# Kernel tuning notes

Measured on AMD Instinct MI355X. Metric: run time of the kernel, lower is better.

The kernel has to match this reference:

```python
import jax, jax.numpy as jnp
import numpy as np

B, N, D, H, DK, DI = 64, 256, 1024, 8, 64, 2048
NEG = -1e9
SCALE = 1.0 / np.sqrt(DK).astype(np.float32)


def _ln(x, s, b, eps=1e-5):
    m = jnp.mean(x, axis=-1, keepdims=True)
    v = jnp.var(x, axis=-1, keepdims=True)
    return (x - m) * jax.lax.rsqrt(v + eps) * s + b


def _glat_basic(x, mask, npm, wq, wk, wv, wo, bo, ls1, lb1, w1, b1, w2, b2, ls2, lb2):
    # mask: [B,1,N,N] bool, True = blocked
    b, n, d = x.shape
    q = (x @ wq).reshape(b, n, H, DK).transpose(0, 2, 1, 3)  # [B,H,N,DK]
    k = (x @ wk).reshape(b, n, H, DK).transpose(0, 2, 1, 3)
    v = (x @ wv).reshape(b, n, H, DK).transpose(0, 2, 1, 3)
    scores = jnp.einsum('bhqd,bhkd->bhqk', q, k) * SCALE
    scores = jnp.where(mask, NEG, scores)
    attn = jax.nn.softmax(scores, axis=-1)
    out = jnp.einsum('bhqk,bhkd->bhqd', attn, v)
    out = out.transpose(0, 2, 1, 3).reshape(b, n, H * DK)
    out = out @ wo + bo
    out = _ln(out + x, ls1, lb1)           # attn residual + layernorm
    out = out * npm                         # non_pad_mask
    h = jax.nn.relu(out @ w1 + b1) @ w2 + b2
    out2 = _ln(h + out, ls2, lb2) * npm     # FFN residual + layernorm + mask
    return out2


def setup_inputs():
    key = jax.random.key(0)
    ks = jax.random.split(key, 40)
    p = lambda i, shape: jax.random.normal(ks[i], shape, jnp.float32) * 0.02
    inp = {
        'x': jax.random.normal(ks[0], (B, N, D), jnp.float32),
        'adj': jax.random.randint(ks[1], (B, N, N), 0, 2).astype(jnp.int32),
        'non_pad_mask': jnp.ones((B, N, 1), jnp.float32),
        'slf_attn_mask': jnp.zeros((B, N, N), jnp.int32),
    }
    i = 2
    for t in ('g', 'l'):
        inp[f'wq_{t}'] = p(i, (D, H * DK)); i += 1
        inp[f'wk_{t}'] = p(i, (D, H * DK)); i += 1
        inp[f'wv_{t}'] = p(i, (D, H * DK)); i += 1
        inp[f'wo_{t}'] = p(i, (H * DK, D)); i += 1
        inp[f'bo_{t}'] = jnp.zeros((D,), jnp.float32)
        inp[f'ln1s_{t}'] = jnp.ones((D,), jnp.float32)
        inp[f'ln1b_{t}'] = jnp.zeros((D,), jnp.float32)
        inp[f'w1_{t}'] = p(i, (D, DI)); i += 1
        inp[f'b1_{t}'] = jnp.zeros((DI,), jnp.float32)
        inp[f'w2_{t}'] = p(i, (DI, D)); i += 1
        inp[f'b2_{t}'] = jnp.zeros((D,), jnp.float32)
        inp[f'ln2s_{t}'] = jnp.ones((D,), jnp.float32)
        inp[f'ln2b_{t}'] = jnp.zeros((D,), jnp.float32)
    inp['fc_w'] = p(i, (2 * D, D)); i += 1
    inp['fc_b'] = jnp.zeros((D,), jnp.float32)
    return inp


def reference(x, adj, non_pad_mask, slf_attn_mask,
              wq_g, wk_g, wv_g, wo_g, bo_g, ln1s_g, ln1b_g, w1_g, b1_g, w2_g, b2_g, ln2s_g, ln2b_g,
              wq_l, wk_l, wv_l, wo_l, bo_l, ln1s_l, ln1b_l, w1_l, b1_l, w2_l, b2_l, ln2s_l, ln2b_l,
              fc_w, fc_b):
    pad_mask = (slf_attn_mask[:, None, :, :] != 0)            # [B,1,N,N]
    local_mask = pad_mask | (adj[:, None, :, :] == 0)         # local: only attend along edges
    x_g = _glat_basic(x, pad_mask, non_pad_mask,
                      wq_g, wk_g, wv_g, wo_g, bo_g, ln1s_g, ln1b_g,
                      w1_g, b1_g, w2_g, b2_g, ln2s_g, ln2b_g)
    x_l = _glat_basic(x, local_mask, non_pad_mask,
                      wq_l, wk_l, wv_l, wo_l, bo_l, ln1s_l, ln1b_l,
                      w1_l, b1_l, w2_l, b2_l, ln2s_l, ln2b_l)
    out = jnp.concatenate([x_g, x_l], axis=-1) @ fc_w + fc_b
    return out
```

## Files before the change

kernel.cpp:

```cpp
#include <hip/hip_runtime.h>


typedef unsigned short u16;
typedef unsigned long long u64;
typedef __bf16 bf16_t;
typedef bf16_t bf16x8 __attribute__((ext_vector_type(8)));
typedef float  f32x4  __attribute__((ext_vector_type(4)));
typedef u16    u16x8  __attribute__((ext_vector_type(8)));
typedef u16    u16x4  __attribute__((ext_vector_type(4)));

__device__ __forceinline__ float bf2f(u16 u){
  union { unsigned int i; float f; } c; c.i = ((unsigned int)u) << 16; return c.f;
}
__device__ __forceinline__ u16 f2bf(float f){
  union { float f; unsigned int u; } c; c.f = f;
  unsigned int u = c.u;
  unsigned int r = (u + 0x7fffu + ((u >> 16) & 1u)) >> 16;
  return (u16)r;
}

__device__ __forceinline__ void gl16(const u16* g, u16* l){
  __builtin_amdgcn_global_load_lds(
      (const __attribute__((address_space(1))) void*)g,
      (__attribute__((address_space(3))) void*)l, 16, 0, 0);
}

__global__ __launch_bounds__(256) void zero_out(float* out, int n){
  for (int i = blockIdx.x * 256 + threadIdx.x; i < n; i += 256 * 4096) out[i] = 0.f;
}

__global__ __launch_bounds__(256) void cvt_bf16(
    const float* __restrict__ in, u16* __restrict__ out)
{
  const size_t i = ((size_t)blockIdx.x * 256 + threadIdx.x) * 8;
  f32x4 a = *(const f32x4*)&in[i];
  f32x4 b = *(const f32x4*)&in[i + 4];
  u16x8 o;
  #pragma unroll
  for (int j = 0; j < 4; ++j){ o[j] = f2bf(a[j]); o[4+j] = f2bf(b[j]); }
  *(u16x8*)&out[i] = o;
}

__global__ __launch_bounds__(256) void transpose_w(
    const float* __restrict__ src, u16* __restrict__ dst, int K, int N, int dstOff)
{
  __shared__ u16 tile[32][33];
  const int bk = blockIdx.x * 32, bn = blockIdx.y * 32;
  const int t = threadIdx.x;
  const int r = t >> 5, c = t & 31;
  #pragma unroll
  for (int p = 0; p < 4; ++p)
    tile[r + p*8][c] = f2bf(src[(size_t)(bk + r + p*8) * N + bn + c]);
  __syncthreads();
  #pragma unroll
  for (int p = 0; p < 4; ++p)
    dst[(size_t)(dstOff + bn + r + p*8) * K + bk + c] = tile[c][r + p*8];
}

template<int RELU, int OF32, int ACC>
__global__ __launch_bounds__(512, 2) void gemm256(
    const u16* __restrict__ A0, const u16* __restrict__ A1,
    int Astride, int ksplit,
    const u16* __restrict__ BT, int Bld, int M, int N, int K,
    const float* __restrict__ bias, void* __restrict__ outv, int out_ld)
{
  __shared__ u16 lds[2*32768];
  const int tid  = threadIdx.x;
  const int lane = tid & 63;
  const int wid  = tid >> 6;
  const int wm = wid >> 2, wn = wid & 3;
  const int l15 = lane & 15, l4 = lane >> 4;
  const int m0 = blockIdx.x * 256, n0 = blockIdx.y * 256;

  f32x4 acc[8][4];
  #pragma unroll
  for (int i = 0; i < 8; ++i)
    #pragma unroll
    for (int j = 0; j < 4; ++j)
      acc[i][j] = (f32x4){0.f, 0.f, 0.f, 0.f};

  const int s0 = tid, s1 = tid + 512;
  const int r0 = s0 >> 3, g0 = (s0 & 7) ^ (r0 & 7);
  const int r1 = s1 >> 3, g1 = (s1 & 7) ^ (r1 & 7);

  const int nt = K >> 6;

  auto stageA = [&](int kt, int h, int buf){
    const int kb = kt * 64;
    const u16* Ab = A0; int kl = kb;
    if (kb >= ksplit){ Ab = A1; kl = kb - ksplit; }
    u16* dst = &lds[buf*32768 + h*8192];
    gl16(&Ab[(size_t)(m0 + h*128 + r0) * Astride + kl + g0*8], &dst[s0*8]);
    gl16(&Ab[(size_t)(m0 + h*128 + r1) * Astride + kl + g1*8], &dst[s1*8]);
  };
  auto stageB = [&](int kt, int h, int buf){
    const int kb = kt * 64;
    u16* dst = &lds[buf*32768 + 16384 + h*8192];
    gl16(&BT[(size_t)(n0 + h*128 + r0) * Bld + kb + g0*8], &dst[s0*8]);
    gl16(&BT[(size_t)(n0 + h*128 + r1) * Bld + kb + g1*8], &dst[s1*8]);
  };
  auto lda = [&](int i, int kc, int buf) -> bf16x8 {
    const int r = wm*128 + i*16 + l15;
    const int c = (kc*4 + l4) ^ (r & 7);
    return *(const bf16x8*)&lds[buf*32768 + r*64 + c*8];
  };
  auto ldb = [&](int j, int kc, int buf) -> bf16x8 {
    const int r = wn*64 + j*16 + l15;
    const int c = (kc*4 + l4) ^ (r & 7);
    return *(const bf16x8*)&lds[buf*32768 + 16384 + r*64 + c*8];
  };

  stageA(0, 0, 0); stageA(0, 1, 0); stageB(0, 0, 0); stageB(0, 1, 0);

  for (int t = 0; t < nt; ++t){
    const int buf = t & 1, nbuf = buf ^ 1;
    const bool pf = (t + 1 < nt);
    if (pf){
      stageA(t+1, 0, nbuf);
      asm volatile("s_waitcnt vmcnt(2)" ::: "memory");
    } else {
      asm volatile("s_waitcnt vmcnt(0)" ::: "memory");
    }
    __builtin_amdgcn_sched_barrier(0);
    __builtin_amdgcn_s_barrier();
    __builtin_amdgcn_sched_barrier(0);

    bf16x8 a_[4][2], b_[2][2];
    #pragma unroll
    for (int i = 0; i < 4; ++i){ a_[i][0] = lda(i, 0, buf); a_[i][1] = lda(i, 1, buf); }
    #pragma unroll
    for (int j = 0; j < 2; ++j){ b_[j][0] = ldb(j, 0, buf); b_[j][1] = ldb(j, 1, buf); }
    if (pf) stageA(t+1, 1, nbuf);
    __builtin_amdgcn_s_setprio(1);
    #pragma unroll
    for (int i = 0; i < 4; ++i)
      #pragma unroll
      for (int j = 0; j < 2; ++j){
        acc[i][j] = __builtin_amdgcn_mfma_f32_16x16x32_bf16(a_[i][0], b_[j][0], acc[i][j], 0,0,0);
        acc[i][j] = __builtin_amdgcn_mfma_f32_16x16x32_bf16(a_[i][1], b_[j][1], acc[i][j], 0,0,0);
      }
    __builtin_amdgcn_s_setprio(0);
    #pragma unroll
    for (int j = 0; j < 2; ++j){ b_[j][0] = ldb(2+j, 0, buf); b_[j][1] = ldb(2+j, 1, buf); }
    if (pf) stageB(t+1, 0, nbuf);
    __builtin_amdgcn_s_setprio(1);
    #pragma unroll
    for (int i = 0; i < 4; ++i)
      #pragma unroll
      for (int j = 0; j < 2; ++j){
        acc[i][2+j] = __builtin_amdgcn_mfma_f32_16x16x32_bf16(a_[i][0], b_[j][0], acc[i][2+j], 0,0,0);
        acc[i][2+j] = __builtin_amdgcn_mfma_f32_16x16x32_bf16(a_[i][1], b_[j][1], acc[i][2+j], 0,0,0);
      }
    __builtin_amdgcn_s_setprio(0);
    #pragma unroll
    for (int i = 0; i < 4; ++i){ a_[i][0] = lda(4+i, 0, buf); a_[i][1] = lda(4+i, 1, buf); }
    if (pf) stageB(t+1, 1, nbuf);
    __builtin_amdgcn_s_setprio(1);
    #pragma unroll
    for (int i = 0; i < 4; ++i)
      #pragma unroll
      for (int j = 0; j < 2; ++j){
        acc[4+i][2+j] = __builtin_amdgcn_mfma_f32_16x16x32_bf16(a_[i][0], b_[j][0], acc[4+i][2+j], 0,0,0);
        acc[4+i][2+j] = __builtin_amdgcn_mfma_f32_16x16x32_bf16(a_[i][1], b_[j][1], acc[4+i][2+j], 0,0,0);
      }
    __builtin_amdgcn_s_setprio(0);
    #pragma unroll
    for (int j = 0; j < 2; ++j){ b_[j][0] = ldb(j, 0, buf); b_[j][1] = ldb(j, 1, buf); }
    __builtin_amdgcn_s_setprio(1);
    #pragma unroll
    for (int i = 0; i < 4; ++i)
      #pragma unroll
      for (int j = 0; j < 2; ++j){
        acc[4+i][j] = __builtin_amdgcn_mfma_f32_16x16x32_bf16(a_[i][0], b_[j][0], acc[4+i][j], 0,0,0);
        acc[4+i][j] = __builtin_amdgcn_mfma_f32_16x16x32_bf16(a_[i][1], b_[j][1], acc[4+i][j], 0,0,0);
      }
    __builtin_amdgcn_s_setprio(0);

    __builtin_amdgcn_sched_barrier(0);
    __builtin_amdgcn_s_barrier();
    __builtin_amdgcn_sched_barrier(0);
  }

  const int rb = m0 + wm*128 + l4*4;
  const int cb = n0 + wn*64 + l15;
  #pragma unroll
  for (int i = 0; i < 8; ++i){
    #pragma unroll
    for (int j = 0; j < 4; ++j){
      const int col = cb + j*16;
      const float badd = bias ? bias[col] : 0.f;
      #pragma unroll
      for (int r = 0; r < 4; ++r){
        const int row = rb + i*16 + r;
        float y = acc[i][j][r] + badd;
        if (RELU) y = y > 0.f ? y : 0.f;
        if (OF32){
          float* po = &((float*)outv)[(size_t)row * out_ld + col];
          if (ACC) y += *po;
          *po = y;
        } else {
          u16* po = &((u16*)outv)[(size_t)row * out_ld + col];
          if (ACC) y += bf2f(*po);
          *po = f2bf(y);
        }
      }
    }
  }
}

__global__ __launch_bounds__(256) void mask_pack(
    const int* __restrict__ slf, const int* __restrict__ adj,
    u64* __restrict__ mb_g, u64* __restrict__ mb_l)
{
  const int idx  = blockIdx.x * 4 + (threadIdx.x >> 6);
  const int lane = threadIdx.x & 63;
  const size_t mi = (size_t)(idx >> 2) * 256 + (size_t)(idx & 3) * 64 + lane;
  const bool g = slf[mi] != 0;
  const bool l = g || (adj[mi] == 0);
  const u64 bg = __ballot(g);
  const u64 bl = __ballot(l);
  if (lane == 0){ mb_g[idx] = bg; mb_l[idx] = bl; }
}

__global__ __launch_bounds__(256) void attn_mfma(
    const u16* __restrict__ qkv, const u64* __restrict__ mb,
    int boff, u16* __restrict__ out)
{
  __shared__ u16 kbuf[64*64];
  __shared__ u16 vtbuf[64*64];
  __shared__ u16 pbuf[4][32*64];

  const int b_loc = blockIdx.x >> 4;
  const int h     = (blockIdx.x >> 1) & 7;
  const int qt    = blockIdx.x & 1;
  const int b     = boff + b_loc;
  const int t     = threadIdx.x;
  const int w     = t >> 6, lane = t & 63;
  const int l15   = lane & 15, l4 = lane >> 4;

  bf16x8 qf[2][2];
  {
    const int rbase = b_loc*256 + qt*128 + w*32;
    #pragma unroll
    for (int i = 0; i < 2; ++i)
      #pragma unroll
      for (int kc = 0; kc < 2; ++kc)
        qf[i][kc] = *(const bf16x8*)&qkv[(size_t)(rbase + i*16 + l15)*1536 + h*64 + kc*32 + l4*8];
  }

  f32x4 acc_o[2][4];
  float m_[2][4], l_[2][4];
  #pragma unroll
  for (int i = 0; i < 2; ++i){
    #pragma unroll
    for (int j = 0; j < 4; ++j) acc_o[i][j] = (f32x4){0.f,0.f,0.f,0.f};
    #pragma unroll
    for (int r = 0; r < 4; ++r){ m_[i][r] = -1e30f; l_[i][r] = 0.f; }
  }

  for (int c = 0; c < 4; ++c){
    __syncthreads();
    {
      const int kr = t >> 2, dg = (t & 3) * 16;
      const size_t rbase = (size_t)(b_loc*256 + c*64 + kr)*1536 + h*64 + dg;
      u16x8 k0 = *(const u16x8*)&qkv[rbase + 512];
      u16x8 k1 = *(const u16x8*)&qkv[rbase + 512 + 8];
      u16x8 v0 = *(const u16x8*)&qkv[rbase + 1024];
      u16x8 v1 = *(const u16x8*)&qkv[rbase + 1024 + 8];
      const int sw = (kr & 7) << 3;
      *(u16x8*)&kbuf[kr*64 + (dg ^ sw)]       = k0;
      *(u16x8*)&kbuf[kr*64 + ((dg + 8) ^ sw)] = k1;
      #pragma unroll
      for (int e = 0; e < 8; ++e){
        const int d0 = dg + e, d1 = dg + 8 + e;
        vtbuf[d0*64 + (kr ^ ((d0 & 7) << 3))] = v0[e];
        vtbuf[d1*64 + (kr ^ ((d1 & 7) << 3))] = v1[e];
      }
    }
    __syncthreads();

    bf16x8 kfr[4][2];
    #pragma unroll
    for (int jb = 0; jb < 4; ++jb){
      const int key = jb*16 + l15;
      const int sw = (key & 7) << 3;
      #pragma unroll
      for (int kc = 0; kc < 2; ++kc)
        kfr[jb][kc] = *(const bf16x8*)&kbuf[key*64 + ((kc*32 + l4*8) ^ sw)];
    }
    f32x4 s_[2][4];
    #pragma unroll
    for (int i = 0; i < 2; ++i)
      #pragma unroll
      for (int jb = 0; jb < 4; ++jb){
        f32x4 a = (f32x4){0.f,0.f,0.f,0.f};
        a = __builtin_amdgcn_mfma_f32_16x16x32_bf16(qf[i][0], kfr[jb][0], a, 0,0,0);
        a = __builtin_amdgcn_mfma_f32_16x16x32_bf16(qf[i][1], kfr[jb][1], a, 0,0,0);
        s_[i][jb] = a;
      }

    #pragma unroll
    for (int i = 0; i < 2; ++i){
      #pragma unroll
      for (int r = 0; r < 4; ++r){
        const int prow = i*16 + l4*4 + r;
        const int qrow = qt*128 + w*32 + prow;
        const u64 bits = mb[((size_t)b*256 + qrow)*4 + c];
        float sv[4];
        #pragma unroll
        for (int jb = 0; jb < 4; ++jb){
          float xv = s_[i][jb][r] * 0.125f;
          if ((bits >> (jb*16 + l15)) & 1ull) xv = -1e9f;
          sv[jb] = xv;
        }
        float mx = fmaxf(fmaxf(sv[0], sv[1]), fmaxf(sv[2], sv[3]));
        #pragma unroll
        for (int d = 1; d < 16; d <<= 1)
          mx = fmaxf(mx, __shfl_xor(mx, d, 64));
        const float mnew = fmaxf(m_[i][r], mx);
        const float corr = __expf(m_[i][r] - mnew);
        m_[i][r] = mnew;
        float ps = 0.f;
        const int swp = (prow & 7) << 3;
        #pragma unroll
        for (int jb = 0; jb < 4; ++jb){
          const float p = __expf(sv[jb] - mnew);
          ps += p;
          pbuf[w][prow*64 + ((jb*16 + l15) ^ swp)] = f2bf(p);
        }
        #pragma unroll
        for (int d = 1; d < 16; d <<= 1)
          ps += __shfl_xor(ps, d, 64);
        l_[i][r] = l_[i][r] * corr + ps;
        #pragma unroll
        for (int j2 = 0; j2 < 4; ++j2) acc_o[i][j2][r] *= corr;
      }
    }

    bf16x8 vfr[4][2];
    #pragma unroll
    for (int j2 = 0; j2 < 4; ++j2){
      const int dim = j2*16 + l15;
      const int sw = (dim & 7) << 3;
      #pragma unroll
      for (int kc = 0; kc < 2; ++kc)
        vfr[j2][kc] = *(const bf16x8*)&vtbuf[dim*64 + ((kc*32 + l4*8) ^ sw)];
    }
    #pragma unroll
    for (int i = 0; i < 2; ++i){
      const int prow = i*16 + l15;
      const int swp = (prow & 7) << 3;
      bf16x8 pa0 = *(const bf16x8*)&pbuf[w][prow*64 + ((l4*8) ^ swp)];
      bf16x8 pa1 = *(const bf16x8*)&pbuf[w][prow*64 + ((32 + l4*8) ^ swp)];
      #pragma unroll
      for (int j2 = 0; j2 < 4; ++j2){
        acc_o[i][j2] = __builtin_amdgcn_mfma_f32_16x16x32_bf16(pa0, vfr[j2][0], acc_o[i][j2], 0,0,0);
        acc_o[i][j2] = __builtin_amdgcn_mfma_f32_16x16x32_bf16(pa1, vfr[j2][1], acc_o[i][j2], 0,0,0);
      }
    }
  }

  #pragma unroll
  for (int i = 0; i < 2; ++i){
    #pragma unroll
    for (int r = 0; r < 4; ++r){
      const int qrow = qt*128 + w*32 + i*16 + l4*4 + r;
      const float inv = 1.f / l_[i][r];
      const size_t ob = ((size_t)b*256 + qrow)*512 + h*64;
      #pragma unroll
      for (int j2 = 0; j2 < 4; ++j2)
        out[ob + j2*16 + l15] = f2bf(acc_o[i][j2][r] * inv);
    }
  }
}

template<int RF32>
__global__ __launch_bounds__(256) void ln_fused(
    const u16* a, const void* __restrict__ res,
    const float* __restrict__ sc, const float* __restrict__ bs,
    const float* __restrict__ npm, u16* out)
{
  const int row = blockIdx.x, t = threadIdx.x;
  const size_t bse = (size_t)row * 1024 + t*4;
  u16x4 av = *(const u16x4*)&a[bse];
  float rv[4];
  if (RF32){
    f32x4 q = *(const f32x4*)&((const float*)res)[bse];
    #pragma unroll
    for (int j = 0; j < 4; ++j) rv[j] = q[j];
  } else {
    u16x4 q = *(const u16x4*)&((const u16*)res)[bse];
    #pragma unroll
    for (int j = 0; j < 4; ++j) rv[j] = bf2f(q[j]);
  }
  float vv[4]; float s = 0.f, sq = 0.f;
  #pragma unroll
  for (int j = 0; j < 4; ++j){
    vv[j] = bf2f(av[j]) + rv[j];
    s += vv[j]; sq += vv[j]*vv[j];
  }
  #pragma unroll
  for (int i = 1; i < 64; i <<= 1){
    s  += __shfl_xor(s,  i, 64);
    sq += __shfl_xor(sq, i, 64);
  }
  __shared__ float red[8];
  const int wid = t >> 6, lane = t & 63;
  if (lane == 0){ red[wid] = s; red[4 + wid] = sq; }
  __syncthreads();
  s  = red[0] + red[1] + red[2] + red[3];
  sq = red[4] + red[5] + red[6] + red[7];
  const float mean = s * (1.f/1024.f);
  const float var  = sq * (1.f/1024.f) - mean*mean;
  const float rstd = rsqrtf(var + 1e-5f);
  const float nm   = npm[row];
  u16x4 ov;
  #pragma unroll
  for (int j = 0; j < 4; ++j){
    float y = (vv[j] - mean) * rstd * sc[t*4+j] + bs[t*4+j];
    ov[j] = f2bf(y * nm);
  }
  *(u16x4*)&out[bse] = ov;
}

extern "C" void kernel_launch(void* const* d_in, const int* in_sizes, int n_in,
                              void* d_out, int out_size, void* d_ws, size_t ws_size,
                              hipStream_t stream)
{
  const size_t NEED = 58720256ull * 2ull;
  if (ws_size < NEED){
    zero_out<<<4096, 256, 0, stream>>>((float*)d_out, out_size);
    return;
  }

  const float* x   = (const float*)d_in[0];
  const int*   adj = (const int*)d_in[1];
  const float* npm = (const float*)d_in[2];
  const int*   slf = (const int*)d_in[3];
  const float* fcw = (const float*)d_in[30];
  const float* fcb = (const float*)d_in[31];

  u16* ws    = (u16*)d_ws;
  u16* wqkvT = ws;
  u16* woT   = ws + 1572864;
  u16* w1T   = ws + 2097152;
  u16* w2T   = ws + 4194304;
  u16* fcT   = ws + 6291456;
  u16* xbf   = ws + 8388608;
  u16* tmp   = ws + 8388608;
  u16* qkvh  = ws + 25165824;
  u16* ln1   = ws + 25165824;
  u16* xg    = ws + 41943040;

  u16* dout16 = (u16*)d_out;
  u16* attnb0 = dout16;
  u16* attnb1 = dout16 + 8388608;
  u16* hbufA  = dout16 + 16777216;
  u64* mb_g   = (u64*)(dout16 + 16777216);
  u64* mb_l   = mb_g + 65536;

  cvt_bf16<<<8192, 256, 0, stream>>>(x, xbf);
  mask_pack<<<16384, 256, 0, stream>>>(slf, adj, mb_g, mb_l);
  transpose_w<<<dim3(64, 32), 256, 0, stream>>>(fcw, fcT, 2048, 1024, 0);

  for (int L = 0; L < 2; ++L){
    const int bi = 4 + L*13;
    transpose_w<<<dim3(32, 16), 256, 0, stream>>>((const float*)d_in[bi+0], wqkvT, 1024, 512, 0);
    transpose_w<<<dim3(32, 16), 256, 0, stream>>>((const float*)d_in[bi+1], wqkvT, 1024, 512, 512);
    transpose_w<<<dim3(32, 16), 256, 0, stream>>>((const float*)d_in[bi+2], wqkvT, 1024, 512, 1024);
    u16* attnb = L ? attnb1 : attnb0;
    for (int hf = 0; hf < 2; ++hf){
      const u16* xh = xbf + (size_t)hf*8192*1024;
      gemm256<0,0,0><<<dim3(32, 6), 512, 0, stream>>>(
          xh, xh, 1024, 1024, wqkvT, 1024, 8192, 1536, 1024, nullptr, qkvh, 1536);
      attn_mfma<<<512, 256, 0, stream>>>(qkvh, L ? mb_l : mb_g, hf*32, attnb);
    }
  }

  for (int L = 0; L < 2; ++L){
    const int bi = 4 + L*13;
    const float* bo  = (const float*)d_in[bi+4];
    const float* l1s = (const float*)d_in[bi+5];
    const float* l1b = (const float*)d_in[bi+6];
    const float* b1  = (const float*)d_in[bi+8];
    const float* b2  = (const float*)d_in[bi+10];
    const float* l2s = (const float*)d_in[bi+11];
    const float* l2b = (const float*)d_in[bi+12];

    transpose_w<<<dim3(16, 32), 256, 0, stream>>>((const float*)d_in[bi+3], woT, 512, 1024, 0);
    transpose_w<<<dim3(32, 64), 256, 0, stream>>>((const float*)d_in[bi+7], w1T, 1024, 2048, 0);
    transpose_w<<<dim3(64, 32), 256, 0, stream>>>((const float*)d_in[bi+9], w2T, 2048, 1024, 0);

    const u16* attnb = L ? attnb1 : attnb0;
    gemm256<0,0,0><<<dim3(64, 4), 512, 0, stream>>>(
        attnb, attnb, 512, 512, woT, 512, 16384, 1024, 512, bo, tmp, 1024);
    ln_fused<1><<<16384, 256, 0, stream>>>(tmp, x, l1s, l1b, npm, ln1);
    for (int hh = 0; hh < 2; ++hh){
      gemm256<1,0,0><<<dim3(64, 4), 512, 0, stream>>>(
          ln1, ln1, 1024, 1024, w1T + (size_t)hh*1024*1024, 1024,
          16384, 1024, 1024, b1 + hh*1024, hbufA, 1024);
      if (hh == 0)
        gemm256<0,0,0><<<dim3(64, 4), 512, 0, stream>>>(
            hbufA, hbufA, 1024, 1024, w2T, 2048, 16384, 1024, 1024, b2, tmp, 1024);
      else
        gemm256<0,0,1><<<dim3(64, 4), 512, 0, stream>>>(
            hbufA, hbufA, 1024, 1024, w2T + 1024, 2048, 16384, 1024, 1024,
            nullptr, tmp, 1024);
    }
    ln_fused<0><<<16384, 256, 0, stream>>>(tmp, ln1, l2s, l2b, npm, L ? tmp : xg);
  }

  gemm256<0,1,0><<<dim3(64, 4), 512, 0, stream>>>(
      xg, tmp, 1024, 1024, fcT, 2048, 16384, 1024, 2048, fcb, d_out, 1024);
}
```

Baseline: 805.2 us.

## Restructure GEMM main loop into barrier-separated phases and merge QKV weight transposes

The gemm256 main loop now puts a workgroup barrier and an explicit lgkmcnt(0) wait around each of its four MFMA sub-phases. The next tile's A and B staging is spread one slice per phase instead of being issued alongside LDS reads, which makes the LDS-read and MFMA interleave across waves more deterministic. The extra barriers add synchronisation cost and may reduce overlap between waves. Separately, the three per-layer Q/K/V weight transpose launches are merged into one launch that picks its source by grid z, saving two kernel launches per layer.

```diff
diff --git a/kernel.cpp b/kernel.cpp
--- a/kernel.cpp
+++ b/kernel.cpp
@@ -45,6 +45,25 @@
     const float* __restrict__ src, u16* __restrict__ dst, int K, int N, int dstOff)
 {
   __shared__ u16 tile[32][33];
+  const int bk = blockIdx.x * 32, bn = blockIdx.y * 32;
+  const int t = threadIdx.x;
+  const int r = t >> 5, c = t & 31;
+  #pragma unroll
+  for (int p = 0; p < 4; ++p)
+    tile[r + p*8][c] = f2bf(src[(size_t)(bk + r + p*8) * N + bn + c]);
+  __syncthreads();
+  #pragma unroll
+  for (int p = 0; p < 4; ++p)
+    dst[(size_t)(dstOff + bn + r + p*8) * K + bk + c] = tile[c][r + p*8];
+}
+
+__global__ __launch_bounds__(256) void transpose_w3(
+    const float* __restrict__ sA, const float* __restrict__ sB,
+    const float* __restrict__ sC, u16* __restrict__ dst, int K, int N)
+{
+  __shared__ u16 tile[32][33];
+  const float* src = blockIdx.z == 0 ? sA : (blockIdx.z == 1 ? sB : sC);
+  const int dstOff = blockIdx.z * N;
   const int bk = blockIdx.x * 32, bn = blockIdx.y * 32;
   const int t = threadIdx.x;
   const int r = t >> 5, c = t & 31;
@@ -110,27 +129,29 @@
     return *(const bf16x8*)&lds[buf*32768 + 16384 + r*64 + c*8];
   };
 
+  #define SBAR  __builtin_amdgcn_sched_barrier(0)
+  #define PBAR  do{ SBAR; __builtin_amdgcn_s_barrier(); SBAR; }while(0)
+  #define LGKM0 do{ asm volatile("s_waitcnt lgkmcnt(0)" ::: "memory"); SBAR; }while(0)
+
   stageA(0, 0, 0); stageA(0, 1, 0); stageB(0, 0, 0); stageB(0, 1, 0);
 
   for (int t = 0; t < nt; ++t){
     const int buf = t & 1, nbuf = buf ^ 1;
     const bool pf = (t + 1 < nt);
+    bf16x8 a_[4][2], b_[2][2];
+
     if (pf){
       stageA(t+1, 0, nbuf);
       asm volatile("s_waitcnt vmcnt(2)" ::: "memory");
     } else {
       asm volatile("s_waitcnt vmcnt(0)" ::: "memory");
     }
-    __builtin_amdgcn_sched_barrier(0);
-    __builtin_amdgcn_s_barrier();
-    __builtin_amdgcn_sched_barrier(0);
-
-    bf16x8 a_[4][2], b_[2][2];
+    PBAR;
     #pragma unroll
     for (int i = 0; i < 4; ++i){ a_[i][0] = lda(i, 0, buf); a_[i][1] = lda(i, 1, buf); }
     #pragma unroll
     for (int j = 0; j < 2; ++j){ b_[j][0] = ldb(j, 0, buf); b_[j][1] = ldb(j, 1, buf); }
-    if (pf) stageA(t+1, 1, nbuf);
+    LGKM0;
     __builtin_amdgcn_s_setprio(1);
     #pragma unroll
     for (int i = 0; i < 4; ++i)
@@ -140,9 +161,12 @@
         acc[i][j] = __builtin_amdgcn_mfma_f32_16x16x32_bf16(a_[i][1], b_[j][1], acc[i][j], 0,0,0);
       }
     __builtin_amdgcn_s_setprio(0);
+    PBAR;
+
     #pragma unroll
     for (int j = 0; j < 2; ++j){ b_[j][0] = ldb(2+j, 0, buf); b_[j][1] = ldb(2+j, 1, buf); }
-    if (pf) stageB(t+1, 0, nbuf);
+    if (pf) stageA(t+1, 1, nbuf);
+    LGKM0;
     __builtin_amdgcn_s_setprio(1);
     #pragma unroll
     for (int i = 0; i < 4; ++i)
@@ -152,9 +176,12 @@
         acc[i][2+j] = __builtin_amdgcn_mfma_f32_16x16x32_bf16(a_[i][1], b_[j][1], acc[i][2+j], 0,0,0);
       }
     __builtin_amdgcn_s_setprio(0);
+    PBAR;
+
     #pragma unroll
     for (int i = 0; i < 4; ++i){ a_[i][0] = lda(4+i, 0, buf); a_[i][1] = lda(4+i, 1, buf); }
-    if (pf) stageB(t+1, 1, nbuf);
+    if (pf) stageB(t+1, 0, nbuf);
+    LGKM0;
     __builtin_amdgcn_s_setprio(1);
     #pragma unroll
     for (int i = 0; i < 4; ++i)
@@ -164,8 +191,12 @@
         acc[4+i][2+j] = __builtin_amdgcn_mfma_f32_16x16x32_bf16(a_[i][1], b_[j][1], acc[4+i][2+j], 0,0,0);
       }
     __builtin_amdgcn_s_setprio(0);
+    PBAR;
+
     #pragma unroll
     for (int j = 0; j < 2; ++j){ b_[j][0] = ldb(j, 0, buf); b_[j][1] = ldb(j, 1, buf); }
+    if (pf) stageB(t+1, 1, nbuf);
+    LGKM0;
     __builtin_amdgcn_s_setprio(1);
     #pragma unroll
     for (int i = 0; i < 4; ++i)
@@ -175,11 +206,11 @@
         acc[4+i][j] = __builtin_amdgcn_mfma_f32_16x16x32_bf16(a_[i][1], b_[j][1], acc[4+i][j], 0,0,0);
       }
     __builtin_amdgcn_s_setprio(0);
-
-    __builtin_amdgcn_sched_barrier(0);
-    __builtin_amdgcn_s_barrier();
-    __builtin_amdgcn_sched_barrier(0);
-  }
+    PBAR;
+  }
+  #undef SBAR
+  #undef PBAR
+  #undef LGKM0
 
   const int rb = m0 + wm*128 + l4*4;
   const int cb = n0 + wn*64 + l15;
@@ -465,9 +496,9 @@
 
   for (int L = 0; L < 2; ++L){
     const int bi = 4 + L*13;
-    transpose_w<<<dim3(32, 16), 256, 0, stream>>>((const float*)d_in[bi+0], wqkvT, 1024, 512, 0);
-    transpose_w<<<dim3(32, 16), 256, 0, stream>>>((const float*)d_in[bi+1], wqkvT, 1024, 512, 512);
-    transpose_w<<<dim3(32, 16), 256, 0, stream>>>((const float*)d_in[bi+2], wqkvT, 1024, 512, 1024);
+    transpose_w3<<<dim3(32, 16, 3), 256, 0, stream>>>(
+        (const float*)d_in[bi+0], (const float*)d_in[bi+1],
+        (const float*)d_in[bi+2], wqkvT, 1024, 512);
     u16* attnb = L ? attnb1 : attnb0;
     for (int hf = 0; hf < 2; ++hf){
       const u16* xh = xbf + (size_t)hf*8192*1024;
```

Measured after the change: 839.8 us. 4.3% more time.
